# Performance work log

Hardware: AMD Instinct MI355X
Metric: run time of the kernel (lower is better)

## Reference

```python
import jax, jax.numpy as jnp
import numpy as np


def _euclidean_cdist(x, q):
    # torch.cdist with p=2: pairwise L2 distances, shape [B, Q]
    x2 = jnp.sum(x * x, axis=-1, keepdims=True)          # [B, 1]
    q2 = jnp.sum(q * q, axis=-1)[None, :]                # [1, Q]
    d2 = x2 + q2 - 2.0 * (x @ q.T)                        # [B, Q]
    return jnp.sqrt(jnp.maximum(d2, 0.0))


def setup_inputs() -> dict:
    key = jax.random.key(0)
    k1, k2 = jax.random.split(key)
    x = jax.random.normal(k1, (1024, 256), dtype=jnp.float32)
    queue = jax.random.normal(k2, (32768, 256), dtype=jnp.float32)
    return {"x": x, "queue": queue}


def reference(x, queue):
    # Queue update: concat then keep the newest max_size rows (queue assumed full)
    max_size = queue.shape[0]
    q = jnp.concatenate([queue, x], axis=0)[-max_size:]   # [Q, F]
    # Distance matrix + top-2 nearest (topk of negated distances)
    d = _euclidean_cdist(x, q)                            # [B, Q]
    _, idx = jax.lax.top_k(-d, 2)                         # [B, 2]
    # Second-nearest neighbor (first is the point itself, dist 0)
    return q[idx[:, 1]]                                   # [B, F]
```

## Files before the change

### kernel.cpp

```cpp
#include <hip/hip_runtime.h>
#include <stdint.h>

#define B_ROWS 1024
#define FEAT   256
#define QSZ    32768
#define SHIFT  1024
#define QX     (QSZ - B_ROWS)
#define BM     64
#define NGY    (QSZ / BM)
#define MARGIN 8.0f

typedef float  v4f __attribute__((ext_vector_type(4)));
typedef short  v8s __attribute__((ext_vector_type(8)));

__device__ __forceinline__ uint32_t key_flip(uint32_t u) {
    return u ^ ((uint32_t)((int32_t)u >> 31) | 0x80000000u);
}
__device__ __forceinline__ float key_m(uint32_t k) {
    uint32_t u = k & 0xFFFF8000u;
    u = (u & 0x80000000u) ? (u ^ 0x80000000u) : ~u;
    return __uint_as_float(u);
}
__device__ __forceinline__ void k2_insert(uint32_t& k1, uint32_t& k2, uint32_t key) {
    uint32_t hi = max(k1, key); k1 = min(k1, key); k2 = min(k2, hi);
}
__device__ __forceinline__ uint2 k2_merge(uint2 a, uint2 b) {
    uint32_t hi = max(a.x, b.x);
    uint2 r; r.x = min(a.x, b.x); r.y = min(min(a.y, b.y), hi);
    return r;
}

struct Top2 { float m1; int j1; float m2; int j2; };
__device__ __forceinline__ bool better(float ma, int ja, float mb, int jb) {
    return (ma < mb) || (ma == mb && ja < jb);
}
__device__ __forceinline__ void t2_insert(Top2& t, float m, int j) {
    if (better(m, j, t.m1, t.j1)) { t.m2 = t.m1; t.j2 = t.j1; t.m1 = m; t.j1 = j; }
    else if (better(m, j, t.m2, t.j2)) { t.m2 = m; t.j2 = j; }
}

__device__ __forceinline__ const float* q_row_ptr(int j, const float* x, const float* queue) {
    return (j < QX) ? (queue + (size_t)(j + SHIFT) * FEAT) : (x + (size_t)(j - QX) * FEAT);
}

__device__ __forceinline__ unsigned short f2bf(float f) {
    uint32_t u = __float_as_uint(f);
    uint32_t r = u + 0x7FFFu + ((u >> 16) & 1u);
    return (unsigned short)(r >> 16);
}

__global__ __launch_bounds__(256) void convert_x(const float* __restrict__ x,
                                                 unsigned short* __restrict__ x_bf) {
    int wave = threadIdx.x >> 6, lane = threadIdx.x & 63;
    int r = blockIdx.x * 4 + wave;
    float4 v = ((const float4*)(x + (size_t)r * FEAT))[lane];
    ushort4 h;
    h.x = f2bf(v.x); h.y = f2bf(v.y); h.z = f2bf(v.z); h.w = f2bf(v.w);
    ((ushort4*)x_bf)[(size_t)r * 64 + lane] = h;
}

__global__ __launch_bounds__(256, 2) void nn_gemm(const float* __restrict__ x,
                                                  const float* __restrict__ queue,
                                                  const unsigned short* __restrict__ x_bf,
                                                  float* __restrict__ q2,
                                                  uint2* __restrict__ partials) {
    __shared__ __align__(16) unsigned short As[BM * FEAT];
    __shared__ __align__(16) float sq2[BM];

    const int t    = threadIdx.x;
    const int w    = t >> 6, lane = t & 63;
    const int quad = lane >> 4, l16 = lane & 15;
    const int gy   = blockIdx.x;

    const unsigned short* bbase = x_bf + (size_t)(w * 256 + l16) * FEAT + quad * 8;
    v8s fb0[8], fb1[8];
#pragma unroll
    for (int kc = 0; kc < 8; ++kc) fb0[kc] = *(const v8s*)(bbase + kc * 32);

    {
        const int arow = t >> 2, aqtr = t & 3;
        const float* asrc = q_row_ptr(gy * BM + arow, x, queue) + aqtr * 64;
        float ss = 0.0f;
#pragma unroll
        for (int gi = 0; gi < 8; ++gi) {
            float4 a = *(const float4*)(asrc + gi * 8);
            float4 b = *(const float4*)(asrc + gi * 8 + 4);
            ss += a.x * a.x + a.y * a.y + a.z * a.z + a.w * a.w
                + b.x * b.x + b.y * b.y + b.z * b.z + b.w * b.w;
            uint32_t p0 = (uint32_t)f2bf(a.x) | ((uint32_t)f2bf(a.y) << 16);
            uint32_t p1 = (uint32_t)f2bf(a.z) | ((uint32_t)f2bf(a.w) << 16);
            uint32_t p2 = (uint32_t)f2bf(b.x) | ((uint32_t)f2bf(b.y) << 16);
            uint32_t p3 = (uint32_t)f2bf(b.z) | ((uint32_t)f2bf(b.w) << 16);
            const int g    = aqtr * 8 + gi;
            const int phys = (g & 24) | ((g & 7) ^ (arow & 7));
            *(uint4*)&As[arow * FEAT + phys * 8] = make_uint4(p0, p1, p2, p3);
        }
        ss += __shfl_xor(ss, 1, 64);
        ss += __shfl_xor(ss, 2, 64);
        if (aqtr == 0) { sq2[arow] = ss; q2[gy * BM + arow] = ss; }
    }

    __syncthreads();

    v8s fa[4][8];
#pragma unroll
    for (int tm = 0; tm < 4; ++tm)
#pragma unroll
        for (int kc = 0; kc < 8; ++kc) {
            const int g  = kc * 4 + quad;
            const int pg = (g & 24) | ((g & 7) ^ (l16 & 7));
            fa[tm][kc] = *(const v8s*)((const char*)As + (size_t)(tm * 16 + l16) * 512 + pg * 16);
        }

    float q2r[4][4];
#pragma unroll
    for (int tm = 0; tm < 4; ++tm) {
        v4f qq = *(const v4f*)&sq2[tm * 16 + quad * 4];
#pragma unroll
        for (int r = 0; r < 4; ++r) q2r[tm][r] = qq[r];
    }

    auto process = [&](int tn, const v8s (&fb)[8]) {
        v4f acc[4] = {(v4f)0.0f, (v4f)0.0f, (v4f)0.0f, (v4f)0.0f};
#pragma unroll
        for (int kc = 0; kc < 8; ++kc)
#pragma unroll
            for (int tm = 0; tm < 4; ++tm)
                acc[tm] = __builtin_amdgcn_mfma_f32_16x16x32_bf16(fa[tm][kc], fb[kc], acc[tm], 0, 0, 0);
        uint32_t k1 = 0xFFFFFFFFu, k2 = 0xFFFFFFFFu;
        const int jb = gy * BM + quad * 4;
#pragma unroll
        for (int tm = 0; tm < 4; ++tm)
#pragma unroll
            for (int r = 0; r < 4; ++r) {
                float m = fmaf(-2.0f, acc[tm][r], q2r[tm][r]);
                uint32_t u = key_flip(__float_as_uint(m));
                uint32_t key = (u & 0xFFFF8000u) | (uint32_t)(jb + tm * 16 + r);
                k2_insert(k1, k2, key);
            }
#pragma unroll
        for (int mask = 16; mask <= 32; mask <<= 1) {
            uint32_t o1 = __shfl_xor(k1, mask, 64);
            uint32_t o2 = __shfl_xor(k2, mask, 64);
            uint32_t hi = max(k1, o1);
            k1 = min(k1, o1);
            k2 = min(min(k2, o2), hi);
        }
        if (quad == 0)
            partials[(size_t)(w * 256 + tn * 16 + l16) * NGY + gy] = make_uint2(k1, k2);
    };

    for (int tp = 0; tp < 8; ++tp) {
        const int tn0 = tp * 2;
#pragma unroll
        for (int kc = 0; kc < 8; ++kc)
            fb1[kc] = *(const v8s*)(bbase + (size_t)(tn0 + 1) * (16 * FEAT) + kc * 32);
        process(tn0, fb0);
        if (tp < 7) {
#pragma unroll
            for (int kc = 0; kc < 8; ++kc)
                fb0[kc] = *(const v8s*)(bbase + (size_t)(tn0 + 2) * (16 * FEAT) + kc * 32);
        }
        process(tn0 + 1, fb1);
    }
}

__global__ __launch_bounds__(256) void nn_finalize(const float* __restrict__ x,
                                                   const float* __restrict__ queue,
                                                   const float* __restrict__ q2,
                                                   const uint2* __restrict__ partials,
                                                   float* __restrict__ out) {
    __shared__ float    xs[256];
    __shared__ uint2    red[256];
    __shared__ int      list[64];
    __shared__ float    escore[64];
    __shared__ int      s_cnt;
    __shared__ uint32_t s_kcut;
    __shared__ int      s_j2;

    const int t = threadIdx.x, i = blockIdx.x;
    const int w = t >> 6, lane = t & 63;

    xs[t] = x[(size_t)i * FEAT + t];
    uint2 pa = partials[(size_t)i * NGY + t];
    uint2 pb = partials[(size_t)i * NGY + 256 + t];
    uint2 pm = k2_merge(pa, pb);
    red[t] = pm;
    if (t == 0) s_cnt = 0;
    __syncthreads();

    if (w == 0) {
        uint2 a = red[lane];
        a = k2_merge(a, red[lane + 64]);
        a = k2_merge(a, red[lane + 128]);
        a = k2_merge(a, red[lane + 192]);
#pragma unroll
        for (int mask = 1; mask <= 32; mask <<= 1) {
            uint2 o;
            o.x = __shfl_xor(a.x, mask, 64);
            o.y = __shfl_xor(a.y, mask, 64);
            a = k2_merge(a, o);
        }
        if (lane == 0) {
            float cutf = key_m(a.y) + MARGIN;
            s_kcut = key_flip(__float_as_uint(cutf)) | 0x7FFFu;
        }
    }
    __syncthreads();
    uint32_t kcut = s_kcut;
    if (pm.x <= kcut) { int q_ = atomicAdd(&s_cnt, 1); if (q_ < 64) list[q_] = (int)(pm.x & 0x7FFFu); }
    if (pm.y <= kcut) { int q_ = atomicAdd(&s_cnt, 1); if (q_ < 64) list[q_] = (int)(pm.y & 0x7FFFu); }
    __syncthreads();
    int n = min(s_cnt, 64);

    for (int c = w; c < n; c += 4) {
        int j = list[c];
        const float4* qr = (const float4*)q_row_ptr(j, x, queue);
        float4 qv = qr[lane];
        float4 xv = ((const float4*)xs)[lane];
        float s = qv.x * xv.x + qv.y * xv.y + qv.z * xv.z + qv.w * xv.w;
#pragma unroll
        for (int off = 32; off; off >>= 1) s += __shfl_xor(s, off, 64);
        if (lane == 0) escore[c] = q2[j] - 2.0f * s;
    }
    __syncthreads();
    if (t == 0) {
        Top2 a;
        a.m1 = __builtin_inff(); a.j1 = 0x7FFFFFFF;
        a.m2 = __builtin_inff(); a.j2 = 0x7FFFFFFF;
        for (int c = 0; c < n; ++c) t2_insert(a, escore[c], list[c]);
        s_j2 = a.j2;
    }
    __syncthreads();
    out[(size_t)i * FEAT + t] = q_row_ptr(s_j2, x, queue)[t];
}

extern "C" void kernel_launch(void* const* d_in, const int* in_sizes, int n_in,
                              void* d_out, int out_size, void* d_ws, size_t ws_size,
                              hipStream_t stream) {
    const float* x     = (const float*)d_in[0];
    const float* queue = (const float*)d_in[1];

    unsigned short* x_bf     = (unsigned short*)d_ws;
    float*          q2       = (float*)((char*)d_ws + (1u << 20));
    uint2*          partials = (uint2*)((char*)d_ws + (2u << 20));

    convert_x<<<B_ROWS / 4, 256, 0, stream>>>(x, x_bf);
    nn_gemm<<<NGY, 256, 0, stream>>>(x, queue, x_bf, q2, partials);
    nn_finalize<<<B_ROWS, 256, 0, stream>>>(x, queue, q2, partials, (float*)d_out);
}
```

Before: 120.7 us.

## Transpose partials layout, split fragment arrays, set MFMA priority, unroll tile loop

The partials buffer is transposed so the GEMM kernel writes contiguous rows per block (gy-major), and the finalize kernel now reads it with a stride of NCOL instead. The A fragments and q2 values move from 2D arrays into separate named registers. The MFMA section is wrapped in s_setprio, and the outer tile loop is fully unrolled. Together these aim to give coalesced partial stores and better instruction scheduling. The cost is strided, uncoalesced reads in finalize and possibly higher register pressure.

Measured after the change: 120.2 us. About the same (-0.4%).

```diff
diff --git a/kernel.cpp b/kernel.cpp
--- a/kernel.cpp
+++ b/kernel.cpp
@@ -8,6 +8,7 @@
 #define QX     (QSZ - B_ROWS)
 #define BM     64
 #define NGY    (QSZ / BM)
+#define NCOL   1024
 #define MARGIN 8.0f
 
 typedef float  v4f __attribute__((ext_vector_type(4)));
@@ -58,6 +59,47 @@
     h.x = f2bf(v.x); h.y = f2bf(v.y); h.z = f2bf(v.z); h.w = f2bf(v.w);
     ((ushort4*)x_bf)[(size_t)r * 64 + lane] = h;
 }
+
+
+#define KEYI(ACC, Q2V, J)                                                  \
+    {                                                                      \
+        float m_ = fmaf(-2.0f, (ACC), (Q2V));                              \
+        uint32_t u_ = key_flip(__float_as_uint(m_));                       \
+        k2_insert(k1, k2, (u_ & 0xFFFF8000u) | (uint32_t)(J));             \
+    }
+
+#define PROCESS(TN, FB)                                                    \
+    {                                                                      \
+        v4f a0 = (v4f)0.0f, a1 = (v4f)0.0f, a2 = (v4f)0.0f, a3 = (v4f)0.0f;\
+        __builtin_amdgcn_s_setprio(1);                                     \
+        _Pragma("unroll")                                                  \
+        for (int kc = 0; kc < 8; ++kc) {                                   \
+            a0 = __builtin_amdgcn_mfma_f32_16x16x32_bf16(fa0[kc], FB[kc], a0, 0, 0, 0); \
+            a1 = __builtin_amdgcn_mfma_f32_16x16x32_bf16(fa1[kc], FB[kc], a1, 0, 0, 0); \
+            a2 = __builtin_amdgcn_mfma_f32_16x16x32_bf16(fa2[kc], FB[kc], a2, 0, 0, 0); \
+            a3 = __builtin_amdgcn_mfma_f32_16x16x32_bf16(fa3[kc], FB[kc], a3, 0, 0, 0); \
+        }                                                                  \
+        __builtin_amdgcn_s_setprio(0);                                     \
+        uint32_t k1 = 0xFFFFFFFFu, k2 = 0xFFFFFFFFu;                       \
+        _Pragma("unroll")                                                  \
+        for (int r = 0; r < 4; ++r) {                                      \
+            KEYI(a0[r], q2r0[r], jb + 0  + r);                             \
+            KEYI(a1[r], q2r1[r], jb + 16 + r);                             \
+            KEYI(a2[r], q2r2[r], jb + 32 + r);                             \
+            KEYI(a3[r], q2r3[r], jb + 48 + r);                             \
+        }                                                                  \
+        _Pragma("unroll")                                                  \
+        for (int mask = 16; mask <= 32; mask <<= 1) {                      \
+            uint32_t o1 = __shfl_xor(k1, mask, 64);                        \
+            uint32_t o2 = __shfl_xor(k2, mask, 64);                        \
+            uint32_t hi = max(k1, o1);                                     \
+            k1 = min(k1, o1);                                              \
+            k2 = min(min(k2, o2), hi);                                     \
+        }                                                                  \
+        if (quad == 0)                                                     \
+            partials[(size_t)gy * NCOL + (w * 256 + (TN) * 16 + l16)] =    \
+                make_uint2(k1, k2);                                        \
+    }
 
 __global__ __launch_bounds__(256, 2) void nn_gemm(const float* __restrict__ x,
                                                   const float* __restrict__ queue,
@@ -102,66 +144,37 @@
 
     __syncthreads();
 
-    v8s fa[4][8];
-#pragma unroll
-    for (int tm = 0; tm < 4; ++tm)
-#pragma unroll
-        for (int kc = 0; kc < 8; ++kc) {
-            const int g  = kc * 4 + quad;
-            const int pg = (g & 24) | ((g & 7) ^ (l16 & 7));
-            fa[tm][kc] = *(const v8s*)((const char*)As + (size_t)(tm * 16 + l16) * 512 + pg * 16);
-        }
-
-    float q2r[4][4];
-#pragma unroll
-    for (int tm = 0; tm < 4; ++tm) {
-        v4f qq = *(const v4f*)&sq2[tm * 16 + quad * 4];
-#pragma unroll
-        for (int r = 0; r < 4; ++r) q2r[tm][r] = qq[r];
-    }
-
-    auto process = [&](int tn, const v8s (&fb)[8]) {
-        v4f acc[4] = {(v4f)0.0f, (v4f)0.0f, (v4f)0.0f, (v4f)0.0f};
-#pragma unroll
-        for (int kc = 0; kc < 8; ++kc)
-#pragma unroll
-            for (int tm = 0; tm < 4; ++tm)
-                acc[tm] = __builtin_amdgcn_mfma_f32_16x16x32_bf16(fa[tm][kc], fb[kc], acc[tm], 0, 0, 0);
-        uint32_t k1 = 0xFFFFFFFFu, k2 = 0xFFFFFFFFu;
-        const int jb = gy * BM + quad * 4;
-#pragma unroll
-        for (int tm = 0; tm < 4; ++tm)
-#pragma unroll
-            for (int r = 0; r < 4; ++r) {
-                float m = fmaf(-2.0f, acc[tm][r], q2r[tm][r]);
-                uint32_t u = key_flip(__float_as_uint(m));
-                uint32_t key = (u & 0xFFFF8000u) | (uint32_t)(jb + tm * 16 + r);
-                k2_insert(k1, k2, key);
-            }
-#pragma unroll
-        for (int mask = 16; mask <= 32; mask <<= 1) {
-            uint32_t o1 = __shfl_xor(k1, mask, 64);
-            uint32_t o2 = __shfl_xor(k2, mask, 64);
-            uint32_t hi = max(k1, o1);
-            k1 = min(k1, o1);
-            k2 = min(min(k2, o2), hi);
-        }
-        if (quad == 0)
-            partials[(size_t)(w * 256 + tn * 16 + l16) * NGY + gy] = make_uint2(k1, k2);
-    };
-
+    v8s fa0[8], fa1[8], fa2[8], fa3[8];
+#pragma unroll
+    for (int kc = 0; kc < 8; ++kc) {
+        const int g  = kc * 4 + quad;
+        const int pg = (g & 24) | ((g & 7) ^ (l16 & 7));
+        const char* rowb = (const char*)As + (size_t)l16 * 512 + pg * 16;
+        fa0[kc] = *(const v8s*)(rowb);
+        fa1[kc] = *(const v8s*)(rowb + 1 * 16 * 512);
+        fa2[kc] = *(const v8s*)(rowb + 2 * 16 * 512);
+        fa3[kc] = *(const v8s*)(rowb + 3 * 16 * 512);
+    }
+
+    v4f q2r0 = *(const v4f*)&sq2[ 0 + quad * 4];
+    v4f q2r1 = *(const v4f*)&sq2[16 + quad * 4];
+    v4f q2r2 = *(const v4f*)&sq2[32 + quad * 4];
+    v4f q2r3 = *(const v4f*)&sq2[48 + quad * 4];
+    const int jb = gy * BM + quad * 4;
+
+#pragma unroll
     for (int tp = 0; tp < 8; ++tp) {
         const int tn0 = tp * 2;
 #pragma unroll
         for (int kc = 0; kc < 8; ++kc)
             fb1[kc] = *(const v8s*)(bbase + (size_t)(tn0 + 1) * (16 * FEAT) + kc * 32);
-        process(tn0, fb0);
+        PROCESS(tn0, fb0);
         if (tp < 7) {
 #pragma unroll
             for (int kc = 0; kc < 8; ++kc)
                 fb0[kc] = *(const v8s*)(bbase + (size_t)(tn0 + 2) * (16 * FEAT) + kc * 32);
         }
-        process(tn0 + 1, fb1);
+        PROCESS(tn0 + 1, fb1);
     }
 }
 
@@ -182,8 +195,8 @@
     const int w = t >> 6, lane = t & 63;
 
     xs[t] = x[(size_t)i * FEAT + t];
-    uint2 pa = partials[(size_t)i * NGY + t];
-    uint2 pb = partials[(size_t)i * NGY + 256 + t];
+    uint2 pa = partials[(size_t)t * NCOL + i];
+    uint2 pb = partials[(size_t)(t + 256) * NCOL + i];
     uint2 pm = k2_merge(pa, pb);
     red[t] = pm;
     if (t == 0) s_cnt = 0;
```
